# Kernel optimization log

Hardware: AMD Instinct MI355X
Metric: run time of the kernel (lower is better)

The kernel has to match this reference:

```python
import jax, jax.numpy as jnp
import numpy as np


def setup_inputs() -> dict:
    key = jax.random.key(0)
    k1, k2, k3, k4 = jax.random.split(key, 4)
    B, S, E, A = 4, 4096, 1024, 1024
    embedded = jax.random.normal(k1, (B, S, E), dtype=jnp.float32)
    # nn.Linear(E, A, bias=False) weights, stored as [E, A] so y = x @ W
    Wk = jax.random.normal(k2, (E, A), dtype=jnp.float32) * (E ** -0.5)
    Wq = jax.random.normal(k3, (E, A), dtype=jnp.float32) * (E ** -0.5)
    Wv = jax.random.normal(k4, (E, A), dtype=jnp.float32) * (E ** -0.5)
    return {"embedded": embedded, "Wk": Wk, "Wq": Wq, "Wv": Wv}


def reference(embedded, Wk, Wq, Wv):
    # K, Q, V projections: [B, S, A]
    K = embedded @ Wk
    Q = embedded @ Wq
    V = embedded @ Wv
    A = K.shape[-1]
    S = embedded.shape[1]
    # causal scores [B, S, S]
    scores = jnp.einsum("bqa,bka->bqk", Q, K) / jnp.sqrt(jnp.float32(A))
    causal = jnp.tril(jnp.ones((S, S), dtype=bool))
    scores = jnp.where(causal, scores, -jnp.inf)
    probs = jax.nn.softmax(scores, axis=-1)
    out = jnp.einsum("bqk,bka->bqa", probs, V)
    # torch.round(out, decimals=4)
    return jnp.round(out, 4)
```

## Files before the change

### kernel.cpp

```cpp
#include <hip/hip_runtime.h>
#include <hip/hip_fp16.h>

typedef __attribute__((ext_vector_type(4))) float f32x4;
typedef __attribute__((ext_vector_type(8))) short s16x8;
typedef __attribute__((ext_vector_type(4))) short s16x4;
typedef unsigned short u16;
typedef unsigned int u32;

__device__ __forceinline__ u16 f2bf(float f) {
    union { float f; unsigned u; } x; x.f = f;
    return (u16)((x.u + 0x7fffu + ((x.u >> 16) & 1u)) >> 16);
}

__device__ __forceinline__ void ld16(const void* g, void* l) {
    __builtin_amdgcn_global_load_lds(
        (const __attribute__((address_space(1))) unsigned int*)g,
        (__attribute__((address_space(3))) unsigned int*)l, 16, 0, 0);
}

__device__ __forceinline__ void kstep2(const u16* gA0, const u16* gA1,
                                       const u16* gB0, const u16* gB1,
                                       const u16* gC0, const u16* gC1,
                                       u16* sA, u16* sB,
                                       int wm, int wn, int lm, int lg, int sx,
                                       f32x4 acc0[4][4], f32x4 acc1[4][4])
{
    const int t = threadIdx.x;
    u16* dA0 = sA + t * 8;        u16* dA1 = sA + 2048 + t * 8;
    u16* dB0 = sB + t * 8;        u16* dB1 = sB + 2048 + t * 8;
    u16* dC0 = sB + 4096 + t * 8; u16* dC1 = sB + 6144 + t * 8;

    __syncthreads();
    ld16(gA0, dA0); ld16(gA1, dA1);
    ld16(gB0, dB0); ld16(gB1, dB1);
    ld16(gC0, dC0); ld16(gC1, dC1);
    __syncthreads();

    s16x8 af[4], bf[4], cf[4];
    const int co = (lg ^ sx) * 8;
#pragma unroll
    for (int i = 0; i < 4; i++) {
        af[i] = *(const s16x8*)&sA[(wm + i * 16 + lm) * 32 + co];
        bf[i] = *(const s16x8*)&sB[(wn + i * 16 + lm) * 32 + co];
        cf[i] = *(const s16x8*)&sB[4096 + (wn + i * 16 + lm) * 32 + co];
    }
#pragma unroll
    for (int i = 0; i < 4; i++)
#pragma unroll
        for (int j = 0; j < 4; j++) {
            acc0[i][j] = __builtin_amdgcn_mfma_f32_16x16x32_bf16(af[i], bf[j], acc0[i][j], 0, 0, 0);
            acc1[i][j] = __builtin_amdgcn_mfma_f32_16x16x32_bf16(af[i], cf[j], acc1[i][j], 0, 0, 0);
        }
}

__device__ __forceinline__ void gemm_core2(const u16* A, long lda,
                                           const u16* B0, const u16* B1, long ldb,
                                           int m0, int kEnd,
                                           f32x4 acc0[4][4], f32x4 acc1[4][4],
                                           u16* sA, u16* sB)
{
    const int t    = threadIdx.x;
    const int lane = t & 63;
    const int wave = t >> 6;
    const int wm   = (wave & 1) << 6;
    const int wn   = (wave >> 1) << 6;
    const int lm   = lane & 15;
    const int lg   = lane >> 4;
    const int sx   = (lm >> 1) & 3;
    const int sr   = t >> 2;
    const int sc   = (((t & 3) ^ ((t >> 3) & 3)) << 3);
    const u16* gA0 = A + (long)(m0 + sr) * lda + sc;
    const u16* gA1 = A + (long)(m0 + 64 + sr) * lda + sc;
    const u16* gB0 = B0 + (long)sr * ldb + sc;
    const u16* gB1 = B0 + (long)(64 + sr) * ldb + sc;
    const u16* gC0 = B1 + (long)sr * ldb + sc;
    const u16* gC1 = B1 + (long)(64 + sr) * ldb + sc;

    for (int k0 = 0; k0 < kEnd; k0 += 32)
        kstep2(gA0 + k0, gA1 + k0, gB0 + k0, gB1 + k0, gC0 + k0, gC1 + k0,
               sA, sB, wm, wn, lm, lg, sx, acc0, acc1);
}

__global__ void convert_x(const float* __restrict__ X, u16* __restrict__ Xb) {
    long idx = ((long)blockIdx.x * 256 + threadIdx.x) * 4;
    f32x4 v = *(const f32x4*)&X[idx];
    s16x4 o;
    o.x = (short)f2bf(v.x); o.y = (short)f2bf(v.y);
    o.z = (short)f2bf(v.z); o.w = (short)f2bf(v.w);
    *(s16x4*)&Xb[idx] = o;
}

__global__ void convert_w(const float* __restrict__ Wk, const float* __restrict__ Wq,
                          const float* __restrict__ Wv,
                          u16* __restrict__ Wkt, u16* __restrict__ Wqt, u16* __restrict__ Wvt) {
    const float* W; u16* O;
    if (blockIdx.y == 0)      { W = Wk; O = Wkt; }
    else if (blockIdx.y == 1) { W = Wq; O = Wqt; }
    else                      { W = Wv; O = Wvt; }
    __shared__ u16 tile[64][65];
    int k0 = (blockIdx.x >> 4) << 6, n0 = (blockIdx.x & 15) << 6;
    int t = threadIdx.x;
    int rr = t >> 4, cc = (t & 15) << 2;
#pragma unroll
    for (int i = 0; i < 4; i++) {
        int row = rr + i * 16;
        f32x4 v = *(const f32x4*)&W[(long)(k0 + row) * 1024 + n0 + cc];
        tile[row][cc + 0] = f2bf(v.x); tile[row][cc + 1] = f2bf(v.y);
        tile[row][cc + 2] = f2bf(v.z); tile[row][cc + 3] = f2bf(v.w);
    }
    __syncthreads();
#pragma unroll
    for (int i = 0; i < 4; i++) {
        int row = rr + i * 16;
        s16x4 pk;
        pk.x = (short)tile[cc + 0][row]; pk.y = (short)tile[cc + 1][row];
        pk.z = (short)tile[cc + 2][row]; pk.w = (short)tile[cc + 3][row];
        *(s16x4*)&O[(long)(n0 + row) * 1024 + k0 + cc] = pk;
    }
}

__global__ __launch_bounds__(256, 2) void proj_all(const u16* __restrict__ X,
                                                   const u16* __restrict__ Wqt,
                                                   const u16* __restrict__ Wkt,
                                                   const u16* __restrict__ Wvt,
                                                   u16* __restrict__ Qb,
                                                   u16* __restrict__ Kb,
                                                   u16* __restrict__ Vt) {
    __shared__ u16 sA[4096], sB[8192];
    int z   = blockIdx.x >> 9;
    int rem = blockIdx.x & 511;
    int m0  = (rem >> 2) * 128;
    int n0  = (rem & 3) * 256;
    const u16* Wt = (z == 0) ? Wqt : (z == 1) ? Wkt : Wvt;

    f32x4 acc0[4][4] = {}, acc1[4][4] = {};
    gemm_core2(X, 1024, Wt + (long)n0 * 1024, Wt + (long)(n0 + 128) * 1024, 1024,
               m0, 1024, acc0, acc1, sA, sB);

    int lane = threadIdx.x & 63, wave = threadIdx.x >> 6;
    int wm = (wave & 1) << 6, wn = (wave >> 1) << 6, lm = lane & 15, lg = lane >> 4;
    if (z < 2) {
        u16* O = (z == 0) ? Qb : Kb;
#pragma unroll
        for (int i = 0; i < 4; i++)
#pragma unroll
            for (int j = 0; j < 4; j++)
#pragma unroll
                for (int r = 0; r < 4; r++) {
                    int row = m0 + wm + i * 16 + lg * 4 + r;
                    int col = n0 + wn + j * 16 + lm;
                    O[(long)row * 1024 + col]       = f2bf(acc0[i][j][r]);
                    O[(long)row * 1024 + col + 128] = f2bf(acc1[i][j][r]);
                }
    } else {
#pragma unroll
        for (int i = 0; i < 4; i++)
#pragma unroll
            for (int j = 0; j < 4; j++) {
                int row0 = m0 + wm + i * 16 + lg * 4;
                int col  = n0 + wn + j * 16 + lm;
                int b = row0 >> 12, s = row0 & 4095;
                s16x4 p0, p1;
                p0.x = (short)f2bf(acc0[i][j][0]); p0.y = (short)f2bf(acc0[i][j][1]);
                p0.z = (short)f2bf(acc0[i][j][2]); p0.w = (short)f2bf(acc0[i][j][3]);
                p1.x = (short)f2bf(acc1[i][j][0]); p1.y = (short)f2bf(acc1[i][j][1]);
                p1.z = (short)f2bf(acc1[i][j][2]); p1.w = (short)f2bf(acc1[i][j][3]);
                *(s16x4*)&Vt[(long)b * 4194304 + (long)col * 4096 + s]         = p0;
                *(s16x4*)&Vt[(long)b * 4194304 + (long)(col + 128) * 4096 + s] = p1;
            }
    }
}

__global__ __launch_bounds__(256, 2) void sgemm_causal(const u16* __restrict__ Q,
                                                       const u16* __restrict__ K,
                                                       u16* __restrict__ S) {
    __shared__ u16 sA[4096], sB[8192];
    int b  = blockIdx.x / 272;
    int tt = blockIdx.x % 272;
    int it = (int)(2.0f * sqrtf((float)tt + 1.0f)) - 1;
    if (it > 31) it = 31;
    if (it < 0) it = 0;
    while (it < 31 && (((it + 2) * (it + 2)) >> 2) <= tt) ++it;
    while (it > 0 && (((it + 1) * (it + 1)) >> 2) > tt) --it;
    int jp  = tt - (((it + 1) * (it + 1)) >> 2);
    int jt0 = jp * 2, jt1 = jt0 + 1;
    bool valid1 = (jt1 <= it);

    const u16* A  = Q + (long)b * 4194304;
    const u16* Kb = K + (long)b * 4194304;
    f32x4 acc0[4][4] = {}, acc1[4][4] = {};
    gemm_core2(A, 1024, Kb + (long)jt0 * 131072, Kb + (long)jt1 * 131072, 1024,
               it * 128, 1024, acc0, acc1, sA, sB);

    long tribase = (long)(b * 528 + ((it * (it + 1)) >> 1));
    u16* Sp0 = S + (tribase + jt0) * 16384;
    u16* Sp1 = S + (tribase + jt1) * 16384;
    int lane = threadIdx.x & 63, wave = threadIdx.x >> 6;
    int wm = (wave & 1) << 6, wn = (wave >> 1) << 6, lm = lane & 15, lg = lane >> 4;
#pragma unroll
    for (int i = 0; i < 4; i++)
#pragma unroll
        for (int j = 0; j < 4; j++)
#pragma unroll
            for (int r = 0; r < 4; r++) {
                int ri = wm + i * 16 + lg * 4 + r;
                int cj = wn + j * 16 + lm;
                int gi = it * 128 + ri;
                float v0 = acc0[i][j][r] * 0.03125f;
                if (jt0 * 128 + cj > gi) v0 = -30000.0f;
                Sp0[ri * 128 + cj] = __half_as_ushort(__float2half(v0));
                if (valid1) {
                    float v1 = acc1[i][j][r] * 0.03125f;
                    if (jt1 * 128 + cj > gi) v1 = -30000.0f;
                    Sp1[ri * 128 + cj] = __half_as_ushort(__float2half(v1));
                }
            }
}

__global__ __launch_bounds__(256) void row_softmax(u16* __restrict__ S,
                                                   float* __restrict__ inv_l) {
    int wave = threadIdx.x >> 6, lane = threadIdx.x & 63;
    int gr = blockIdx.x * 4 + wave;
    int b  = gr >> 12;
    int r  = gr & 4095;
    int it = r >> 7, ri = r & 127;
    u16* base = S + (long)(b * 528 + ((it * (it + 1)) >> 1)) * 16384 + ri * 128;
    int c = lane * 2;

    float m = -1e30f;
    for (int jt = 0; jt <= it; jt++) {
        u32 v = *(const u32*)&base[jt * 16384 + c];
        float a0 = __half2float(__ushort_as_half((u16)(v & 0xffff)));
        float a1 = __half2float(__ushort_as_half((u16)(v >> 16)));
        m = fmaxf(m, fmaxf(a0, a1));
    }
#pragma unroll
    for (int o = 32; o; o >>= 1) m = fmaxf(m, __shfl_xor(m, o, 64));

    const float LOG2E = 1.44269504088896f;
    float l = 0.0f;
    for (int jt = 0; jt <= it; jt++) {
        u32 v = *(const u32*)&base[jt * 16384 + c];
        float a0 = __half2float(__ushort_as_half((u16)(v & 0xffff)));
        float a1 = __half2float(__ushort_as_half((u16)(v >> 16)));
        float p0 = exp2f((a0 - m) * LOG2E);
        float p1 = exp2f((a1 - m) * LOG2E);
        u32 o = (u32)f2bf(p0) | ((u32)f2bf(p1) << 16);
        *(u32*)&base[jt * 16384 + c] = o;
        l += p0 + p1;
    }
#pragma unroll
    for (int o = 32; o; o >>= 1) l += __shfl_xor(l, o, 64);
    if (lane == 0) inv_l[gr] = 1.0f / l;
}

__global__ __launch_bounds__(256, 2) void pv_gemm(const u16* __restrict__ P,
                                                  const u16* __restrict__ Vt,
                                                  const float* __restrict__ inv_l,
                                                  float* __restrict__ Out) {
    __shared__ u16 sA[4096], sB[8192];
    int g  = blockIdx.x;
    int it = (g < 256) ? (31 - (g >> 4)) : ((g - 256) >> 4);
    int rem = g & 15;
    int b   = rem >> 2;
    int atp = rem & 3;

    const int t    = threadIdx.x;
    const int lane = t & 63;
    const int wave = t >> 6;
    const int wm   = (wave & 1) << 6;
    const int wn   = (wave >> 1) << 6;
    const int lm   = lane & 15;
    const int lg   = lane >> 4;
    const int sx   = (lm >> 1) & 3;
    const int sr   = t >> 2;
    const int sc   = (((t & 3) ^ ((t >> 3) & 3)) << 3);

    const u16* Pbase = P + (long)(b * 528 + ((it * (it + 1)) >> 1)) * 16384;
    const u16* gA0 = Pbase + sr * 128 + sc;
    const u16* gA1 = gA0 + 64 * 128;
    const u16* gB0 = Vt + (long)b * 4194304 + (long)(atp * 256 + sr) * 4096 + sc;
    const u16* gB1 = gB0 + (long)64 * 4096;
    const u16* gC0 = gB0 + (long)128 * 4096;
    const u16* gC1 = gB0 + (long)192 * 4096;

    f32x4 acc0[4][4] = {}, acc1[4][4] = {};
    for (int jt = 0; jt <= it; jt++) {
        long aoff = (long)jt * 16384;
        long boff = (long)jt * 128;
#pragma unroll
        for (int kk = 0; kk < 128; kk += 32)
            kstep2(gA0 + aoff + kk, gA1 + aoff + kk,
                   gB0 + boff + kk, gB1 + boff + kk,
                   gC0 + boff + kk, gC1 + boff + kk,
                   sA, sB, wm, wn, lm, lg, sx, acc0, acc1);
    }

#pragma unroll
    for (int i = 0; i < 4; i++)
#pragma unroll
        for (int j = 0; j < 4; j++)
#pragma unroll
            for (int r = 0; r < 4; r++) {
                int gi = it * 128 + wm + i * 16 + lg * 4 + r;
                int ga = atp * 256 + wn + j * 16 + lm;
                float s = inv_l[b * 4096 + gi];
                Out[((long)b * 4096 + gi) * 1024 + ga]       = acc0[i][j][r] * s;
                Out[((long)b * 4096 + gi) * 1024 + ga + 128] = acc1[i][j][r] * s;
            }
}

extern "C" void kernel_launch(void* const* d_in, const int* in_sizes, int n_in,
                              void* d_out, int out_size, void* d_ws, size_t ws_size,
                              hipStream_t stream) {
    const float* X  = (const float*)d_in[0];
    const float* Wk = (const float*)d_in[1];
    const float* Wq = (const float*)d_in[2];
    const float* Wv = (const float*)d_in[3];
    float* Out = (float*)d_out;

    char* w = (char*)d_ws;
    u16*   Qb   = (u16*)(w);
    u16*   Kb   = (u16*)(w + 33554432);
    u16*   Vt   = (u16*)(w + 67108864);
    float* invl = (float*)(w + 100663296);
    u16*   Xb   = (u16*)(w + 100728832);
    u16*   Wqt  = (u16*)(w + 134283264);
    u16*   Wkt  = (u16*)(w + 136380416);
    u16*   Wvt  = (u16*)(w + 138477568);
    u16*   S    = (u16*)(w + 100728832);

    convert_x<<<16384, 256, 0, stream>>>(X, Xb);
    convert_w<<<dim3(256, 3), 256, 0, stream>>>(Wk, Wq, Wv, Wkt, Wqt, Wvt);
    proj_all<<<1536, 256, 0, stream>>>(Xb, Wqt, Wkt, Wvt, Qb, Kb, Vt);
    sgemm_causal<<<1088, 256, 0, stream>>>(Qb, Kb, S);
    row_softmax<<<4096, 256, 0, stream>>>(S, invl);
    pv_gemm<<<512, 256, 0, stream>>>(S, Vt, invl, Out);
}
```

Measured before the change: 496.5 us.

## Double-buffer LDS with register prefetch in all GEMM kernels

Replaces the single-buffered global_load_lds k-step, which had two barriers per step, with a software pipeline. The next k-slice is loaded into registers while MFMAs run on the current LDS buffer, then stored into the alternate buffer, leaving one barrier per step. LDS per block doubles to 48 KB, and register pressure rises under launch_bounds(256,2), which could cause spills or cut occupancy. Row_softmax also now walks rows in reverse order, presumably so the longest rows are scheduled first.

```diff
diff --git a/kernel.cpp b/kernel.cpp
--- a/kernel.cpp
+++ b/kernel.cpp
@@ -12,52 +12,10 @@
     return (u16)((x.u + 0x7fffu + ((x.u >> 16) & 1u)) >> 16);
 }
 
-__device__ __forceinline__ void ld16(const void* g, void* l) {
-    __builtin_amdgcn_global_load_lds(
-        (const __attribute__((address_space(1))) unsigned int*)g,
-        (__attribute__((address_space(3))) unsigned int*)l, 16, 0, 0);
-}
-
-__device__ __forceinline__ void kstep2(const u16* gA0, const u16* gA1,
-                                       const u16* gB0, const u16* gB1,
-                                       const u16* gC0, const u16* gC1,
-                                       u16* sA, u16* sB,
-                                       int wm, int wn, int lm, int lg, int sx,
-                                       f32x4 acc0[4][4], f32x4 acc1[4][4])
-{
-    const int t = threadIdx.x;
-    u16* dA0 = sA + t * 8;        u16* dA1 = sA + 2048 + t * 8;
-    u16* dB0 = sB + t * 8;        u16* dB1 = sB + 2048 + t * 8;
-    u16* dC0 = sB + 4096 + t * 8; u16* dC1 = sB + 6144 + t * 8;
-
-    __syncthreads();
-    ld16(gA0, dA0); ld16(gA1, dA1);
-    ld16(gB0, dB0); ld16(gB1, dB1);
-    ld16(gC0, dC0); ld16(gC1, dC1);
-    __syncthreads();
-
-    s16x8 af[4], bf[4], cf[4];
-    const int co = (lg ^ sx) * 8;
-#pragma unroll
-    for (int i = 0; i < 4; i++) {
-        af[i] = *(const s16x8*)&sA[(wm + i * 16 + lm) * 32 + co];
-        bf[i] = *(const s16x8*)&sB[(wn + i * 16 + lm) * 32 + co];
-        cf[i] = *(const s16x8*)&sB[4096 + (wn + i * 16 + lm) * 32 + co];
-    }
-#pragma unroll
-    for (int i = 0; i < 4; i++)
-#pragma unroll
-        for (int j = 0; j < 4; j++) {
-            acc0[i][j] = __builtin_amdgcn_mfma_f32_16x16x32_bf16(af[i], bf[j], acc0[i][j], 0, 0, 0);
-            acc1[i][j] = __builtin_amdgcn_mfma_f32_16x16x32_bf16(af[i], cf[j], acc1[i][j], 0, 0, 0);
-        }
-}
-
-__device__ __forceinline__ void gemm_core2(const u16* A, long lda,
-                                           const u16* B0, const u16* B1, long ldb,
-                                           int m0, int kEnd,
-                                           f32x4 acc0[4][4], f32x4 acc1[4][4],
-                                           u16* sA, u16* sB)
+template <typename AddrF>
+__device__ __forceinline__ void gemm_pipe(int nsteps, AddrF addr,
+                                          f32x4 acc0[4][4], f32x4 acc1[4][4],
+                                          u16* sA, u16* sB)
 {
     const int t    = threadIdx.x;
     const int lane = t & 63;
@@ -66,19 +24,54 @@
     const int wn   = (wave >> 1) << 6;
     const int lm   = lane & 15;
     const int lg   = lane >> 4;
-    const int sx   = (lm >> 1) & 3;
-    const int sr   = t >> 2;
-    const int sc   = (((t & 3) ^ ((t >> 3) & 3)) << 3);
-    const u16* gA0 = A + (long)(m0 + sr) * lda + sc;
-    const u16* gA1 = A + (long)(m0 + 64 + sr) * lda + sc;
-    const u16* gB0 = B0 + (long)sr * ldb + sc;
-    const u16* gB1 = B0 + (long)(64 + sr) * ldb + sc;
-    const u16* gC0 = B1 + (long)sr * ldb + sc;
-    const u16* gC1 = B1 + (long)(64 + sr) * ldb + sc;
-
-    for (int k0 = 0; k0 < kEnd; k0 += 32)
-        kstep2(gA0 + k0, gA1 + k0, gB0 + k0, gB1 + k0, gC0 + k0, gC1 + k0,
-               sA, sB, wm, wn, lm, lg, sx, acc0, acc1);
+    const int co   = (lg ^ ((lm >> 1) & 3)) * 8;
+
+    const u16 *pa0, *pa1, *pb0, *pb1, *pc0, *pc1;
+    addr(0, pa0, pa1, pb0, pb1, pc0, pc1);
+    s16x8 ra0 = *(const s16x8*)pa0, ra1 = *(const s16x8*)pa1;
+    s16x8 rb0 = *(const s16x8*)pb0, rb1 = *(const s16x8*)pb1;
+    s16x8 rc0 = *(const s16x8*)pc0, rc1 = *(const s16x8*)pc1;
+    {
+        u16* wA = sA + t * 8;
+        u16* wB = sB + t * 8;
+        *(s16x8*)(wA)        = ra0; *(s16x8*)(wA + 2048) = ra1;
+        *(s16x8*)(wB)        = rb0; *(s16x8*)(wB + 2048) = rb1;
+        *(s16x8*)(wB + 4096) = rc0; *(s16x8*)(wB + 6144) = rc1;
+    }
+    __syncthreads();
+
+    for (int k = 0; k < nsteps; ++k) {
+        const int kb = k & 1, nb = kb ^ 1;
+        const int kn = (k + 1 < nsteps) ? (k + 1) : k;
+        addr(kn, pa0, pa1, pb0, pb1, pc0, pc1);
+        ra0 = *(const s16x8*)pa0; ra1 = *(const s16x8*)pa1;
+        rb0 = *(const s16x8*)pb0; rb1 = *(const s16x8*)pb1;
+        rc0 = *(const s16x8*)pc0; rc1 = *(const s16x8*)pc1;
+
+        const u16* bA = sA + kb * 4096;
+        const u16* bB = sB + kb * 8192;
+        s16x8 af[4], bf[4], cf[4];
+#pragma unroll
+        for (int i = 0; i < 4; i++) {
+            af[i] = *(const s16x8*)&bA[(wm + i * 16 + lm) * 32 + co];
+            bf[i] = *(const s16x8*)&bB[(wn + i * 16 + lm) * 32 + co];
+            cf[i] = *(const s16x8*)&bB[4096 + (wn + i * 16 + lm) * 32 + co];
+        }
+#pragma unroll
+        for (int i = 0; i < 4; i++)
+#pragma unroll
+            for (int j = 0; j < 4; j++) {
+                acc0[i][j] = __builtin_amdgcn_mfma_f32_16x16x32_bf16(af[i], bf[j], acc0[i][j], 0, 0, 0);
+                acc1[i][j] = __builtin_amdgcn_mfma_f32_16x16x32_bf16(af[i], cf[j], acc1[i][j], 0, 0, 0);
+            }
+
+        u16* qA = sA + nb * 4096 + t * 8;
+        u16* qB = sB + nb * 8192 + t * 8;
+        *(s16x8*)(qA)        = ra0; *(s16x8*)(qA + 2048) = ra1;
+        *(s16x8*)(qB)        = rb0; *(s16x8*)(qB + 2048) = rb1;
+        *(s16x8*)(qB + 4096) = rc0; *(s16x8*)(qB + 6144) = rc1;
+        __syncthreads();
+    }
 }
 
 __global__ void convert_x(const float* __restrict__ X, u16* __restrict__ Xb) {
@@ -126,18 +119,34 @@
                                                    u16* __restrict__ Qb,
                                                    u16* __restrict__ Kb,
                                                    u16* __restrict__ Vt) {
-    __shared__ u16 sA[4096], sB[8192];
+    __shared__ u16 sA[8192], sB[16384];
     int z   = blockIdx.x >> 9;
     int rem = blockIdx.x & 511;
     int m0  = (rem >> 2) * 128;
     int n0  = (rem & 3) * 256;
     const u16* Wt = (z == 0) ? Wqt : (z == 1) ? Wkt : Wvt;
 
+    const int t  = threadIdx.x;
+    const int sr = t >> 2;
+    const int sc = (((t & 3) ^ ((t >> 3) & 3)) << 3);
+    const u16* gA0 = X + (long)(m0 + sr) * 1024 + sc;
+    const u16* gA1 = gA0 + (long)64 * 1024;
+    const u16* gB0 = Wt + (long)(n0 + sr) * 1024 + sc;
+    const u16* gB1 = gB0 + (long)64 * 1024;
+    const u16* gC0 = gB0 + (long)128 * 1024;
+    const u16* gC1 = gB0 + (long)192 * 1024;
+
     f32x4 acc0[4][4] = {}, acc1[4][4] = {};
-    gemm_core2(X, 1024, Wt + (long)n0 * 1024, Wt + (long)(n0 + 128) * 1024, 1024,
-               m0, 1024, acc0, acc1, sA, sB);
-
-    int lane = threadIdx.x & 63, wave = threadIdx.x >> 6;
+    auto addr = [&](int k, const u16*& a0, const u16*& a1, const u16*& b0,
+                    const u16*& b1, const u16*& c0, const u16*& c1) {
+        int off = k << 5;
+        a0 = gA0 + off; a1 = gA1 + off;
+        b0 = gB0 + off; b1 = gB1 + off;
+        c0 = gC0 + off; c1 = gC1 + off;
+    };
+    gemm_pipe(32, addr, acc0, acc1, sA, sB);
+
+    int lane = t & 63, wave = t >> 6;
     int wm = (wave & 1) << 6, wn = (wave >> 1) << 6, lm = lane & 15, lg = lane >> 4;
     if (z < 2) {
         u16* O = (z == 0) ? Qb : Kb;
@@ -174,7 +183,7 @@
 __global__ __launch_bounds__(256, 2) void sgemm_causal(const u16* __restrict__ Q,
                                                        const u16* __restrict__ K,
                                                        u16* __restrict__ S) {
-    __shared__ u16 sA[4096], sB[8192];
+    __shared__ u16 sA[8192], sB[16384];
     int b  = blockIdx.x / 272;
     int tt = blockIdx.x % 272;
     int it = (int)(2.0f * sqrtf((float)tt + 1.0f)) - 1;
@@ -187,15 +196,32 @@
     bool valid1 = (jt1 <= it);
 
     const u16* A  = Q + (long)b * 4194304;
-    const u16* Kb = K + (long)b * 4194304;
+    const u16* Kp = K + (long)b * 4194304;
+
+    const int t  = threadIdx.x;
+    const int sr = t >> 2;
+    const int sc = (((t & 3) ^ ((t >> 3) & 3)) << 3);
+    const u16* gA0 = A + (long)(it * 128 + sr) * 1024 + sc;
+    const u16* gA1 = gA0 + (long)64 * 1024;
+    const u16* gB0 = Kp + (long)(jt0 * 128 + sr) * 1024 + sc;
+    const u16* gB1 = gB0 + (long)64 * 1024;
+    const u16* gC0 = Kp + (long)(jt1 * 128 + sr) * 1024 + sc;
+    const u16* gC1 = gC0 + (long)64 * 1024;
+
     f32x4 acc0[4][4] = {}, acc1[4][4] = {};
-    gemm_core2(A, 1024, Kb + (long)jt0 * 131072, Kb + (long)jt1 * 131072, 1024,
-               it * 128, 1024, acc0, acc1, sA, sB);
+    auto addr = [&](int k, const u16*& a0, const u16*& a1, const u16*& b0,
+                    const u16*& b1, const u16*& c0, const u16*& c1) {
+        int off = k << 5;
+        a0 = gA0 + off; a1 = gA1 + off;
+        b0 = gB0 + off; b1 = gB1 + off;
+        c0 = gC0 + off; c1 = gC1 + off;
+    };
+    gemm_pipe(32, addr, acc0, acc1, sA, sB);
 
     long tribase = (long)(b * 528 + ((it * (it + 1)) >> 1));
     u16* Sp0 = S + (tribase + jt0) * 16384;
     u16* Sp1 = S + (tribase + jt1) * 16384;
-    int lane = threadIdx.x & 63, wave = threadIdx.x >> 6;
+    int lane = t & 63, wave = t >> 6;
     int wm = (wave & 1) << 6, wn = (wave >> 1) << 6, lm = lane & 15, lg = lane >> 4;
 #pragma unroll
     for (int i = 0; i < 4; i++)
@@ -220,7 +246,7 @@
 __global__ __launch_bounds__(256) void row_softmax(u16* __restrict__ S,
                                                    float* __restrict__ inv_l) {
     int wave = threadIdx.x >> 6, lane = threadIdx.x & 63;
-    int gr = blockIdx.x * 4 + wave;
+    int gr = 16383 - (blockIdx.x * 4 + wave);
     int b  = gr >> 12;
     int r  = gr & 4095;
     int it = r >> 7, ri = r & 127;
@@ -258,23 +284,16 @@
                                                   const u16* __restrict__ Vt,
                                                   const float* __restrict__ inv_l,
                                                   float* __restrict__ Out) {
-    __shared__ u16 sA[4096], sB[8192];
+    __shared__ u16 sA[8192], sB[16384];
     int g  = blockIdx.x;
     int it = (g < 256) ? (31 - (g >> 4)) : ((g - 256) >> 4);
     int rem = g & 15;
     int b   = rem >> 2;
     int atp = rem & 3;
 
-    const int t    = threadIdx.x;
-    const int lane = t & 63;
-    const int wave = t >> 6;
-    const int wm   = (wave & 1) << 6;
-    const int wn   = (wave >> 1) << 6;
-    const int lm   = lane & 15;
-    const int lg   = lane >> 4;
-    const int sx   = (lm >> 1) & 3;
-    const int sr   = t >> 2;
-    const int sc   = (((t & 3) ^ ((t >> 3) & 3)) << 3);
+    const int t  = threadIdx.x;
+    const int sr = t >> 2;
+    const int sc = (((t & 3) ^ ((t >> 3) & 3)) << 3);
 
     const u16* Pbase = P + (long)(b * 528 + ((it * (it + 1)) >> 1)) * 16384;
     const u16* gA0 = Pbase + sr * 128 + sc;
@@ -285,17 +304,19 @@
     const u16* gC1 = gB0 + (long)192 * 4096;
 
     f32x4 acc0[4][4] = {}, acc1[4][4] = {};
-    for (int jt = 0; jt <= it; jt++) {
-        long aoff = (long)jt * 16384;
-        long boff = (long)jt * 128;
-#pragma unroll
-        for (int kk = 0; kk < 128; kk += 32)
-            kstep2(gA0 + aoff + kk, gA1 + aoff + kk,
-                   gB0 + boff + kk, gB1 + boff + kk,
-                   gC0 + boff + kk, gC1 + boff + kk,
-                   sA, sB, wm, wn, lm, lg, sx, acc0, acc1);
-    }
-
+    auto addr = [&](int k, const u16*& a0, const u16*& a1, const u16*& b0,
+                    const u16*& b1, const u16*& c0, const u16*& c1) {
+        int jt = k >> 2, kk = (k & 3) << 5;
+        long aoff = (long)jt * 16384 + kk;
+        long boff = (long)jt * 128 + kk;
+        a0 = gA0 + aoff; a1 = gA1 + aoff;
+        b0 = gB0 + boff; b1 = gB1 + boff;
+        c0 = gC0 + boff; c1 = gC1 + boff;
+    };
+    gemm_pipe((it + 1) * 4, addr, acc0, acc1, sA, sB);
+
+    int lane = t & 63, wave = t >> 6;
+    int wm = (wave & 1) << 6, wn = (wave >> 1) << 6, lm = lane & 15, lg = lane >> 4;
 #pragma unroll
     for (int i = 0; i < 4; i++)
 #pragma unroll
```

Measured after the change: 491.1 us. No clear change (-1.1%).
